# Kernel optimization log

Measured on AMD Instinct MI355X. Metric: run time of the kernel, lower is better.

## Reference

```python
import jax, jax.numpy as jnp
import numpy as np

HID = 768          # args.hidden_size
LSTM2 = 768        # args.lstm_dim * 2
SCALE = HID ** -0.5


def _cross_attn(q_in, kv_in, Wq, bq, Wk, bk, Wv, bv):
    # Linear projections (weights stored as [in, out])
    Q = q_in @ Wq + bq            # [B, Sq, H]
    K = kv_in @ Wk + bk           # [B, Sk, H]
    V = kv_in @ Wv + bv           # [B, Sk, H]
    attn = jnp.einsum('bqh,bkh->bqk', Q, K) * SCALE
    attn = jax.nn.softmax(attn, axis=-1)
    return jnp.einsum('bqk,bkh->bqh', attn, V)


def setup_inputs() -> dict:
    key = jax.random.key(0)
    ks = jax.random.split(key, 14)
    B, Ssyn, Ssem = 4, 4096, 2048
    syntactic_feat = jax.random.normal(ks[0], (B, Ssyn, LSTM2), jnp.float32)
    semantic_feat = jax.random.normal(ks[1], (B, Ssem, HID), jnp.float32)

    def lin(k, fan_in, fan_out):
        kw, kb = jax.random.split(k)
        bound = 1.0 / np.sqrt(fan_in)
        W = jax.random.uniform(kw, (fan_in, fan_out), jnp.float32, -bound, bound)
        b = jax.random.uniform(kb, (fan_out,), jnp.float32, -bound, bound)
        return W, b

    # syntax_to_semantic: query_dim=HID, key_dim=LSTM2
    Wq1, bq1 = lin(ks[2], HID, HID)
    Wk1, bk1 = lin(ks[3], LSTM2, HID)
    Wv1, bv1 = lin(ks[4], LSTM2, HID)
    # semantic_to_syntax: query_dim=LSTM2, key_dim=HID
    Wq2, bq2 = lin(ks[5], LSTM2, HID)
    Wk2, bk2 = lin(ks[6], HID, HID)
    Wv2, bv2 = lin(ks[7], HID, HID)
    return dict(syntactic_feat=syntactic_feat, semantic_feat=semantic_feat,
                Wq1=Wq1, bq1=bq1, Wk1=Wk1, bk1=bk1, Wv1=Wv1, bv1=bv1,
                Wq2=Wq2, bq2=bq2, Wk2=Wk2, bk2=bk2, Wv2=Wv2, bv2=bv2)


def reference(syntactic_feat, semantic_feat,
              Wq1, bq1, Wk1, bk1, Wv1, bv1,
              Wq2, bq2, Wk2, bk2, Wv2, bv2):
    # enhanced_semantic: queries from semantic, keys/values from syntactic
    enhanced_semantic = _cross_attn(semantic_feat, syntactic_feat,
                                    Wq1, bq1, Wk1, bk1, Wv1, bv1)
    # enhanced_syntax: queries from syntactic, keys/values from semantic
    enhanced_syntax = _cross_attn(syntactic_feat, semantic_feat,
                                  Wq2, bq2, Wk2, bk2, Wv2, bv2)
    return enhanced_semantic, enhanced_syntax
```

## Files before the change

kernel.cpp:

```cpp
#include <hip/hip_runtime.h>
#include <stdint.h>


typedef unsigned short u16;
typedef __attribute__((ext_vector_type(8))) __bf16 bf16x8;
typedef __attribute__((ext_vector_type(4))) float f32x4;

__device__ __forceinline__ float bf2f(u16 u) {
  union { unsigned int i; float f; } x; x.i = ((unsigned int)u) << 16; return x.f;
}
__device__ __forceinline__ u16 f2bf(float f) {
  union { float f; unsigned int i; } x; x.f = f;
  unsigned int i = x.i;
  i += 0x7fffu + ((i >> 16) & 1u);
  return (u16)(i >> 16);
}

__device__ __forceinline__ void cp16(void* lds, const void* g) {
  __builtin_amdgcn_global_load_lds((__attribute__((address_space(1))) void*)g,
                                   (__attribute__((address_space(3))) void*)lds,
                                   16, 0, 0);
}

template <int BIAS_MODE, int OUTF>
__global__ __launch_bounds__(256)
void gemm_bt_kernel(const u16* __restrict__ A, const u16* __restrict__ Bt,
                    const float* __restrict__ bias, void* __restrict__ Cv,
                    int K, int lda, int ldb, int ldc,
                    long sAb, long sBb, long sCb, float scale)
{
  __shared__ __align__(16) u16 Asl[128 * 32];
  __shared__ __align__(16) u16 Bsl[128 * 32];

  const int tid  = threadIdx.x;
  const int lane = tid & 63;
  const int wave = tid >> 6;
  const int l15  = lane & 15;
  const int quad = lane >> 4;
  const int mw   = (wave >> 1) * 64;
  const int nw   = (wave & 1) * 64;

  const long zb = blockIdx.z;
  const char* Ab = (const char*)(A + zb * sAb + (long)blockIdx.x * 128 * lda);
  const char* Bb = (const char*)(Bt + zb * sBb + (long)blockIdx.y * 128 * ldb);

  const int o   = wave * 1024 + lane * 16;
  const int mst = o >> 6;
  const int off = o & 63;
  char* ldsA = (char*)Asl + wave * 1024;
  char* ldsB = (char*)Bsl + wave * 1024;
  const long ldaB = (long)lda * 2;
  const long ldbB = (long)ldb * 2;
  const char* pa0 = Ab + (long)mst * ldaB + off;
  const char* pb0 = Bb + (long)mst * ldbB + off;

  f32x4 acc[4][4];
  {
    f32x4 zz = {0.f, 0.f, 0.f, 0.f};
#pragma unroll
    for (int i = 0; i < 4; ++i)
#pragma unroll
      for (int j = 0; j < 4; ++j) acc[i][j] = zz;
  }

  const int nk = K >> 5;
  for (int kk = 0; kk < nk; ++kk) {
    const long kb = (long)kk << 6;
    cp16(ldsA,        pa0 + kb);
    cp16(ldsA + 4096, pa0 + kb + 64 * ldaB);
    cp16(ldsB,        pb0 + kb);
    cp16(ldsB + 4096, pb0 + kb + 64 * ldbB);
    __syncthreads();

    bf16x8 a[4], b[4];
    const bf16x8* As8 = (const bf16x8*)Asl;
    const bf16x8* Bs8 = (const bf16x8*)Bsl;
#pragma unroll
    for (int i = 0; i < 4; ++i) a[i] = As8[(mw + i * 16 + l15) * 4 + quad];
#pragma unroll
    for (int j = 0; j < 4; ++j) b[j] = Bs8[(nw + j * 16 + l15) * 4 + quad];
#pragma unroll
    for (int i = 0; i < 4; ++i)
#pragma unroll
      for (int j = 0; j < 4; ++j)
        acc[i][j] = __builtin_amdgcn_mfma_f32_16x16x32_bf16(a[i], b[j], acc[i][j], 0, 0, 0);
    __syncthreads();
  }

  const int brow = blockIdx.x * 128 + mw + quad * 4;
  const int bcol = blockIdx.y * 128 + nw + l15;
  float cb[4];
  if (BIAS_MODE == 1) {
#pragma unroll
    for (int j = 0; j < 4; ++j) cb[j] = bias[bcol + j * 16];
  }
#pragma unroll
  for (int i = 0; i < 4; ++i) {
    const int r0 = brow + i * 16;
    float rb[4];
    if (BIAS_MODE == 2) {
#pragma unroll
      for (int r = 0; r < 4; ++r) rb[r] = bias[r0 + r];
    }
#pragma unroll
    for (int j = 0; j < 4; ++j) {
      const int col = bcol + j * 16;
#pragma unroll
      for (int r = 0; r < 4; ++r) {
        float x = acc[i][j][r] * scale;
        if (BIAS_MODE == 1) x += cb[j];
        if (BIAS_MODE == 2) x += rb[r];
        if (OUTF)
          ((float*)Cv)[zb * sCb + (long)(r0 + r) * ldc + col] = x;
        else
          ((u16*)Cv)[zb * sCb + (long)(r0 + r) * ldc + col] = f2bf(x);
      }
    }
  }
}

__global__ __launch_bounds__(256)
void cvt_bf16_kernel(const float* __restrict__ src, u16* __restrict__ dst, int n8)
{
  int idx = blockIdx.x * 256 + threadIdx.x;
  if (idx >= n8) return;
  const float4* s4 = (const float4*)src;
  float4 a = s4[idx * 2], b = s4[idx * 2 + 1];
  uint4 o;
  o.x = (unsigned int)f2bf(a.x) | ((unsigned int)f2bf(a.y) << 16);
  o.y = (unsigned int)f2bf(a.z) | ((unsigned int)f2bf(a.w) << 16);
  o.z = (unsigned int)f2bf(b.x) | ((unsigned int)f2bf(b.y) << 16);
  o.w = (unsigned int)f2bf(b.z) | ((unsigned int)f2bf(b.w) << 16);
  ((uint4*)dst)[idx] = o;
}

__global__ void transpose6_kernel(const float* s0, const float* s1, const float* s2,
                                  const float* s3, const float* s4, const float* s5,
                                  u16* d0, u16* d1, u16* d2,
                                  u16* d3, u16* d4, u16* d5)
{
  __shared__ float t[32][33];
  const float* src; u16* dst;
  switch (blockIdx.z) {
    case 0: src = s0; dst = d0; break;
    case 1: src = s1; dst = d1; break;
    case 2: src = s2; dst = d2; break;
    case 3: src = s3; dst = d3; break;
    case 4: src = s4; dst = d4; break;
    default: src = s5; dst = d5; break;
  }
  const int tx = threadIdx.x, ty = threadIdx.y;
  const int x = blockIdx.x * 32 + tx;
  const int y0 = blockIdx.y * 32;
#pragma unroll
  for (int j = 0; j < 32; j += 8) t[ty + j][tx] = src[(long)(y0 + ty + j) * 768 + x];
  __syncthreads();
  const int x2 = y0 + tx;
#pragma unroll
  for (int j = 0; j < 32; j += 8)
    dst[(long)(blockIdx.x * 32 + ty + j) * 768 + x2] = f2bf(t[tx][ty + j]);
}

template <int NV>
__global__ __launch_bounds__(256)
void softmax_kernel(u16* S)
{
  __shared__ float red[8];
  const int tid  = threadIdx.x;
  const int lane = tid & 63;
  const int wave = tid >> 6;
  uint4* p4 = (uint4*)(S + (long)blockIdx.x * (NV * 256));

  uint4 ld[NV / 8];
#pragma unroll
  for (int c = 0; c < NV / 8; ++c) ld[c] = p4[tid + c * 256];
  float v[NV];
#pragma unroll
  for (int c = 0; c < NV / 8; ++c) {
    unsigned int w[4] = {ld[c].x, ld[c].y, ld[c].z, ld[c].w};
#pragma unroll
    for (int q = 0; q < 4; ++q) {
      v[c * 8 + q * 2]     = bf2f((u16)(w[q] & 0xffffu));
      v[c * 8 + q * 2 + 1] = bf2f((u16)(w[q] >> 16));
    }
  }

  float m = -1e30f;
#pragma unroll
  for (int i = 0; i < NV; ++i) m = fmaxf(m, v[i]);
#pragma unroll
  for (int off = 32; off > 0; off >>= 1) m = fmaxf(m, __shfl_xor(m, off, 64));
  if (lane == 0) red[wave] = m;
  __syncthreads();
  m = fmaxf(fmaxf(red[0], red[1]), fmaxf(red[2], red[3]));

  float s = 0.f;
#pragma unroll
  for (int i = 0; i < NV; ++i) { v[i] = __expf(v[i] - m); s += v[i]; }
#pragma unroll
  for (int off = 32; off > 0; off >>= 1) s += __shfl_xor(s, off, 64);
  if (lane == 0) red[4 + wave] = s;
  __syncthreads();
  s = (red[4] + red[5]) + (red[6] + red[7]);
  const float inv = 1.0f / s;

#pragma unroll
  for (int c = 0; c < NV / 8; ++c) {
    unsigned int w[4];
#pragma unroll
    for (int q = 0; q < 4; ++q) {
      const u16 lo = f2bf(v[c * 8 + q * 2] * inv);
      const u16 hi = f2bf(v[c * 8 + q * 2 + 1] * inv);
      w[q] = (unsigned int)lo | ((unsigned int)hi << 16);
    }
    uint4 st; st.x = w[0]; st.y = w[1]; st.z = w[2]; st.w = w[3];
    p4[tid + c * 256] = st;
  }
}


static void launch_gemm(hipStream_t st, int mode, int outf,
                        const void* A, const void* Bt, const float* bias, void* C,
                        int M, int N, int K, int lda, int ldb, int ldc,
                        long sA, long sB, long sC, int nb, float scale)
{
  dim3 g(M / 128, N / 128, nb), b(256, 1, 1);
  const u16* Au = (const u16*)A;
  const u16* Bu = (const u16*)Bt;
  if (outf == 0) {
    if (mode == 0)
      gemm_bt_kernel<0, 0><<<g, b, 0, st>>>(Au, Bu, bias, C, K, lda, ldb, ldc, sA, sB, sC, scale);
    else if (mode == 1)
      gemm_bt_kernel<1, 0><<<g, b, 0, st>>>(Au, Bu, bias, C, K, lda, ldb, ldc, sA, sB, sC, scale);
    else
      gemm_bt_kernel<2, 0><<<g, b, 0, st>>>(Au, Bu, bias, C, K, lda, ldb, ldc, sA, sB, sC, scale);
  } else {
    if (mode == 0)
      gemm_bt_kernel<0, 1><<<g, b, 0, st>>>(Au, Bu, bias, C, K, lda, ldb, ldc, sA, sB, sC, scale);
    else if (mode == 1)
      gemm_bt_kernel<1, 1><<<g, b, 0, st>>>(Au, Bu, bias, C, K, lda, ldb, ldc, sA, sB, sC, scale);
    else
      gemm_bt_kernel<2, 1><<<g, b, 0, st>>>(Au, Bu, bias, C, K, lda, ldb, ldc, sA, sB, sC, scale);
  }
}

extern "C" void kernel_launch(void* const* d_in, const int* in_sizes, int n_in,
                              void* d_out, int out_size, void* d_ws, size_t ws_size,
                              hipStream_t stream)
{
  (void)in_sizes; (void)n_in; (void)out_size; (void)ws_size;
  const float* syn = (const float*)d_in[0];
  const float* sem = (const float*)d_in[1];
  const float* W[6]    = {(const float*)d_in[2], (const float*)d_in[4],  (const float*)d_in[6],
                          (const float*)d_in[8], (const float*)d_in[10], (const float*)d_in[12]};
  const float* bias[6] = {(const float*)d_in[3], (const float*)d_in[5],  (const float*)d_in[7],
                          (const float*)d_in[9], (const float*)d_in[11], (const float*)d_in[13]};
  float* out = (float*)d_out;

  u16* ws   = (u16*)d_ws;
  u16* WT   = ws;
  u16* synb = ws + 3538944;
  u16* semb = synb + 12582912;
  u16* bufA = semb + 6291456;
  u16* bufB = bufA + 12582912;
  u16* bufC = bufB + 12582912;
  u16* S    = bufC + 6291456;

  const float SC = 0.036084391824351615f;

  cvt_bf16_kernel<<<dim3(6144), dim3(256), 0, stream>>>(syn, synb, 1572864);
  cvt_bf16_kernel<<<dim3(3072), dim3(256), 0, stream>>>(sem, semb, 786432);
  transpose6_kernel<<<dim3(24, 24, 6), dim3(32, 8, 1), 0, stream>>>(
      W[0], W[1], W[2], W[3], W[4], W[5],
      WT + 0 * 589824, WT + 1 * 589824, WT + 2 * 589824,
      WT + 3 * 589824, WT + 4 * 589824, WT + 5 * 589824);

  launch_gemm(stream, 1, 0, synb, WT + 1 * 589824, bias[1], bufA,
              16384, 768, 768, 768, 768, 768, 0, 0, 0, 1, 1.f);
  launch_gemm(stream, 2, 0, WT + 2 * 589824, synb, bias[2], bufB,
              768, 16384, 768, 768, 768, 16384, 0, 0, 0, 1, 1.f);
  launch_gemm(stream, 1, 0, semb, WT + 0 * 589824, bias[0], bufC,
              8192, 768, 768, 768, 768, 768, 0, 0, 0, 1, 1.f);
  launch_gemm(stream, 0, 0, bufC, bufA, nullptr, S,
              2048, 4096, 768, 768, 768, 4096,
              2048L * 768, 4096L * 768, 2048L * 4096, 4, SC);
  softmax_kernel<16><<<dim3(8192), dim3(256), 0, stream>>>(S);
  launch_gemm(stream, 0, 1, S, bufB, nullptr, out,
              2048, 768, 4096, 4096, 16384, 768,
              2048L * 4096, 4096L, 2048L * 768, 4, 1.f);

  launch_gemm(stream, 1, 0, synb, WT + 3 * 589824, bias[3], bufA,
              16384, 768, 768, 768, 768, 768, 0, 0, 0, 1, 1.f);
  launch_gemm(stream, 1, 0, semb, WT + 4 * 589824, bias[4], bufC,
              8192, 768, 768, 768, 768, 768, 0, 0, 0, 1, 1.f);
  launch_gemm(stream, 2, 0, WT + 5 * 589824, semb, bias[5], bufB,
              768, 8192, 768, 768, 768, 8192, 0, 0, 0, 1, 1.f);
  launch_gemm(stream, 0, 0, bufA, bufC, nullptr, S,
              4096, 2048, 768, 768, 768, 2048,
              4096L * 768, 2048L * 768, 4096L * 2048, 4, SC);
  softmax_kernel<8><<<dim3(16384), dim3(256), 0, stream>>>(S);
  launch_gemm(stream, 0, 1, S, bufB, nullptr, out + 6291456,
              4096, 768, 2048, 2048, 8192, 768,
              4096L * 2048, 2048L, 4096L * 768, 4, 1.f);
}
```

Before: 703.6 us.

## Batch independent GEMMs into grouped multi-descriptor launches and merge conversion kernels

Replaces the templated GEMM with a grouped kernel that reads a pack of GEMM descriptors and maps a flat block index to the right problem. All six projections go in one launch, the second attention's QK^T shares a launch with the first attention's PV GEMM, and the two fp32-to-bf16 conversions are fused into one kernel. Workspace is reshuffled, and some intermediates are staged in the output buffer. The goal is fewer launches and better fill of the GPU with small GEMMs. In exchange, bias mode and output type become runtime branches instead of template parameters, which may add register pressure or instructions.

```diff
diff --git a/kernel.cpp b/kernel.cpp
--- a/kernel.cpp
+++ b/kernel.cpp
@@ -22,15 +22,34 @@
                                    16, 0, 0);
 }
 
-template <int BIAS_MODE, int OUTF>
+struct GemmDesc {
+  const u16* A; const u16* Bt; const float* bias; void* C;
+  long sA, sB, sC;
+  int K, lda, ldb, ldc;
+  int gx, gy;
+  int start;
+  int mode, outf;
+  float scale;
+};
+struct GemmPack { GemmDesc d[6]; int nd; };
+
 __global__ __launch_bounds__(256)
-void gemm_bt_kernel(const u16* __restrict__ A, const u16* __restrict__ Bt,
-                    const float* __restrict__ bias, void* __restrict__ Cv,
-                    int K, int lda, int ldb, int ldc,
-                    long sAb, long sBb, long sCb, float scale)
+void gemm_multi_kernel(GemmPack p)
 {
   __shared__ __align__(16) u16 Asl[128 * 32];
   __shared__ __align__(16) u16 Bsl[128 * 32];
+
+  int seg = 0;
+#pragma unroll
+  for (int t = 1; t < 6; ++t)
+    if (t < p.nd && (int)blockIdx.x >= p.d[t].start) seg = t;
+  const GemmDesc& g = p.d[seg];
+  const int local = (int)blockIdx.x - g.start;
+  const int pxy = g.gx * g.gy;
+  const int bz = local / pxy;
+  const int rem = local - bz * pxy;
+  const int by = rem / g.gx;
+  const int bx = rem - by * g.gx;
 
   const int tid  = threadIdx.x;
   const int lane = tid & 63;
@@ -40,17 +59,16 @@
   const int mw   = (wave >> 1) * 64;
   const int nw   = (wave & 1) * 64;
 
-  const long zb = blockIdx.z;
-  const char* Ab = (const char*)(A + zb * sAb + (long)blockIdx.x * 128 * lda);
-  const char* Bb = (const char*)(Bt + zb * sBb + (long)blockIdx.y * 128 * ldb);
+  const char* Ab = (const char*)(g.A + (long)bz * g.sA + (long)bx * 128 * g.lda);
+  const char* Bb = (const char*)(g.Bt + (long)bz * g.sB + (long)by * 128 * g.ldb);
 
   const int o   = wave * 1024 + lane * 16;
   const int mst = o >> 6;
   const int off = o & 63;
   char* ldsA = (char*)Asl + wave * 1024;
   char* ldsB = (char*)Bsl + wave * 1024;
-  const long ldaB = (long)lda * 2;
-  const long ldbB = (long)ldb * 2;
+  const long ldaB = (long)g.lda * 2;
+  const long ldbB = (long)g.ldb * 2;
   const char* pa0 = Ab + (long)mst * ldaB + off;
   const char* pb0 = Bb + (long)mst * ldbB + off;
 
@@ -63,7 +81,7 @@
       for (int j = 0; j < 4; ++j) acc[i][j] = zz;
   }
 
-  const int nk = K >> 5;
+  const int nk = g.K >> 5;
   for (int kk = 0; kk < nk; ++kk) {
     const long kb = (long)kk << 6;
     cp16(ldsA,        pa0 + kb);
@@ -87,51 +105,53 @@
     __syncthreads();
   }
 
-  const int brow = blockIdx.x * 128 + mw + quad * 4;
-  const int bcol = blockIdx.y * 128 + nw + l15;
+  const int brow = bx * 128 + mw + quad * 4;
+  const int bcol = by * 128 + nw + l15;
   float cb[4];
-  if (BIAS_MODE == 1) {
-#pragma unroll
-    for (int j = 0; j < 4; ++j) cb[j] = bias[bcol + j * 16];
+  if (g.mode == 1) {
+#pragma unroll
+    for (int j = 0; j < 4; ++j) cb[j] = g.bias[bcol + j * 16];
   }
 #pragma unroll
   for (int i = 0; i < 4; ++i) {
     const int r0 = brow + i * 16;
     float rb[4];
-    if (BIAS_MODE == 2) {
-#pragma unroll
-      for (int r = 0; r < 4; ++r) rb[r] = bias[r0 + r];
+    if (g.mode == 2) {
+#pragma unroll
+      for (int r = 0; r < 4; ++r) rb[r] = g.bias[r0 + r];
     }
 #pragma unroll
     for (int j = 0; j < 4; ++j) {
       const int col = bcol + j * 16;
 #pragma unroll
       for (int r = 0; r < 4; ++r) {
-        float x = acc[i][j][r] * scale;
-        if (BIAS_MODE == 1) x += cb[j];
-        if (BIAS_MODE == 2) x += rb[r];
-        if (OUTF)
-          ((float*)Cv)[zb * sCb + (long)(r0 + r) * ldc + col] = x;
-        else
-          ((u16*)Cv)[zb * sCb + (long)(r0 + r) * ldc + col] = f2bf(x);
+        float x = acc[i][j][r] * g.scale;
+        if (g.mode == 1) x += cb[j];
+        if (g.mode == 2) x += rb[r];
+        const long idx = (long)bz * g.sC + (long)(r0 + r) * g.ldc + col;
+        if (g.outf) ((float*)g.C)[idx] = x;
+        else        ((u16*)g.C)[idx] = f2bf(x);
       }
     }
   }
 }
 
 __global__ __launch_bounds__(256)
-void cvt_bf16_kernel(const float* __restrict__ src, u16* __restrict__ dst, int n8)
+void cvt2_bf16_kernel(const float* __restrict__ sa, u16* __restrict__ da, int n8a,
+                      const float* __restrict__ sb, u16* __restrict__ db, int n8b)
 {
   int idx = blockIdx.x * 256 + threadIdx.x;
-  if (idx >= n8) return;
+  const float* src; u16* dst; int i;
+  if (idx < n8a) { src = sa; dst = da; i = idx; }
+  else           { src = sb; dst = db; i = idx - n8a; if (i >= n8b) return; }
   const float4* s4 = (const float4*)src;
-  float4 a = s4[idx * 2], b = s4[idx * 2 + 1];
+  float4 a = s4[i * 2], b = s4[i * 2 + 1];
   uint4 o;
   o.x = (unsigned int)f2bf(a.x) | ((unsigned int)f2bf(a.y) << 16);
   o.y = (unsigned int)f2bf(a.z) | ((unsigned int)f2bf(a.w) << 16);
   o.z = (unsigned int)f2bf(b.x) | ((unsigned int)f2bf(b.y) << 16);
   o.w = (unsigned int)f2bf(b.z) | ((unsigned int)f2bf(b.w) << 16);
-  ((uint4*)dst)[idx] = o;
+  ((uint4*)dst)[i] = o;
 }
 
 __global__ void transpose6_kernel(const float* s0, const float* s1, const float* s2,
@@ -219,29 +239,18 @@
 }
 
 
-static void launch_gemm(hipStream_t st, int mode, int outf,
-                        const void* A, const void* Bt, const float* bias, void* C,
-                        int M, int N, int K, int lda, int ldb, int ldc,
-                        long sA, long sB, long sC, int nb, float scale)
-{
-  dim3 g(M / 128, N / 128, nb), b(256, 1, 1);
-  const u16* Au = (const u16*)A;
-  const u16* Bu = (const u16*)Bt;
-  if (outf == 0) {
-    if (mode == 0)
-      gemm_bt_kernel<0, 0><<<g, b, 0, st>>>(Au, Bu, bias, C, K, lda, ldb, ldc, sA, sB, sC, scale);
-    else if (mode == 1)
-      gemm_bt_kernel<1, 0><<<g, b, 0, st>>>(Au, Bu, bias, C, K, lda, ldb, ldc, sA, sB, sC, scale);
-    else
-      gemm_bt_kernel<2, 0><<<g, b, 0, st>>>(Au, Bu, bias, C, K, lda, ldb, ldc, sA, sB, sC, scale);
-  } else {
-    if (mode == 0)
-      gemm_bt_kernel<0, 1><<<g, b, 0, st>>>(Au, Bu, bias, C, K, lda, ldb, ldc, sA, sB, sC, scale);
-    else if (mode == 1)
-      gemm_bt_kernel<1, 1><<<g, b, 0, st>>>(Au, Bu, bias, C, K, lda, ldb, ldc, sA, sB, sC, scale);
-    else
-      gemm_bt_kernel<2, 1><<<g, b, 0, st>>>(Au, Bu, bias, C, K, lda, ldb, ldc, sA, sB, sC, scale);
-  }
+static GemmDesc mkdesc(const void* A, const void* Bt, const float* bias, void* C,
+                       long sA, long sB, long sC, int K, int lda, int ldb, int ldc,
+                       int M, int N, int nb, int start, int mode, int outf, float scale)
+{
+  GemmDesc d;
+  d.A = (const u16*)A; d.Bt = (const u16*)Bt; d.bias = bias; d.C = C;
+  d.sA = sA; d.sB = sB; d.sC = sC;
+  d.K = K; d.lda = lda; d.ldb = ldb; d.ldc = ldc;
+  d.gx = M / 128; d.gy = N / 128; d.start = start;
+  d.mode = mode; d.outf = outf; d.scale = scale;
+  (void)nb;
+  return d;
 }
 
 extern "C" void kernel_launch(void* const* d_in, const int* in_sizes, int n_in,
@@ -260,46 +269,71 @@
   u16* ws   = (u16*)d_ws;
   u16* WT   = ws;
   u16* synb = ws + 3538944;
-  u16* semb = synb + 12582912;
-  u16* bufA = semb + 6291456;
-  u16* bufB = bufA + 12582912;
-  u16* bufC = bufB + 12582912;
-  u16* S    = bufC + 6291456;
+  u16* semb = ws + 16121856;
+  u16* S1   = ws;
+  u16* K1   = ws + 33554432;
+  u16* Q1   = ws + 46137344;
+  u16* S2   = ws + 33554432;
+  u16* V1T  = ws + 67108864;
+  u16* V2T  = ws + 79691776;
+  u16* Q2   = (u16*)(out + 6291456);
+  u16* K2   = Q2 + 12582912;
 
   const float SC = 0.036084391824351615f;
 
-  cvt_bf16_kernel<<<dim3(6144), dim3(256), 0, stream>>>(syn, synb, 1572864);
-  cvt_bf16_kernel<<<dim3(3072), dim3(256), 0, stream>>>(sem, semb, 786432);
+  cvt2_bf16_kernel<<<dim3(9216), dim3(256), 0, stream>>>(
+      syn, synb, 1572864, sem, semb, 786432);
+
   transpose6_kernel<<<dim3(24, 24, 6), dim3(32, 8, 1), 0, stream>>>(
       W[0], W[1], W[2], W[3], W[4], W[5],
       WT + 0 * 589824, WT + 1 * 589824, WT + 2 * 589824,
       WT + 3 * 589824, WT + 4 * 589824, WT + 5 * 589824);
 
-  launch_gemm(stream, 1, 0, synb, WT + 1 * 589824, bias[1], bufA,
-              16384, 768, 768, 768, 768, 768, 0, 0, 0, 1, 1.f);
-  launch_gemm(stream, 2, 0, WT + 2 * 589824, synb, bias[2], bufB,
-              768, 16384, 768, 768, 768, 16384, 0, 0, 0, 1, 1.f);
-  launch_gemm(stream, 1, 0, semb, WT + 0 * 589824, bias[0], bufC,
-              8192, 768, 768, 768, 768, 768, 0, 0, 0, 1, 1.f);
-  launch_gemm(stream, 0, 0, bufC, bufA, nullptr, S,
-              2048, 4096, 768, 768, 768, 4096,
-              2048L * 768, 4096L * 768, 2048L * 4096, 4, SC);
-  softmax_kernel<16><<<dim3(8192), dim3(256), 0, stream>>>(S);
-  launch_gemm(stream, 0, 1, S, bufB, nullptr, out,
-              2048, 768, 4096, 4096, 16384, 768,
-              2048L * 4096, 4096L, 2048L * 768, 4, 1.f);
-
-  launch_gemm(stream, 1, 0, synb, WT + 3 * 589824, bias[3], bufA,
-              16384, 768, 768, 768, 768, 768, 0, 0, 0, 1, 1.f);
-  launch_gemm(stream, 1, 0, semb, WT + 4 * 589824, bias[4], bufC,
-              8192, 768, 768, 768, 768, 768, 0, 0, 0, 1, 1.f);
-  launch_gemm(stream, 2, 0, WT + 5 * 589824, semb, bias[5], bufB,
-              768, 8192, 768, 768, 768, 8192, 0, 0, 0, 1, 1.f);
-  launch_gemm(stream, 0, 0, bufA, bufC, nullptr, S,
-              4096, 2048, 768, 768, 768, 2048,
-              4096L * 768, 2048L * 768, 4096L * 2048, 4, SC);
-  softmax_kernel<8><<<dim3(16384), dim3(256), 0, stream>>>(S);
-  launch_gemm(stream, 0, 1, S, bufB, nullptr, out + 6291456,
-              4096, 768, 2048, 2048, 8192, 768,
-              4096L * 2048, 2048L, 4096L * 768, 4, 1.f);
-}
+  {
+    GemmPack p; p.nd = 6;
+    p.d[0] = mkdesc(synb, WT + 1 * 589824, bias[1], K1, 0, 0, 0,
+                    768, 768, 768, 768, 16384, 768, 1, 0, 1, 0, 1.f);
+    p.d[1] = mkdesc(synb, WT + 3 * 589824, bias[3], Q2, 0, 0, 0,
+                    768, 768, 768, 768, 16384, 768, 1, 768, 1, 0, 1.f);
+    p.d[2] = mkdesc(WT + 2 * 589824, synb, bias[2], V1T, 0, 0, 0,
+                    768, 768, 768, 16384, 768, 16384, 1, 1536, 2, 0, 1.f);
+    p.d[3] = mkdesc(semb, WT + 0 * 589824, bias[0], Q1, 0, 0, 0,
+                    768, 768, 768, 768, 8192, 768, 1, 2304, 1, 0, 1.f);
+    p.d[4] = mkdesc(semb, WT + 4 * 589824, bias[4], K2, 0, 0, 0,
+                    768, 768, 768, 768, 8192, 768, 1, 2688, 1, 0, 1.f);
+    p.d[5] = mkdesc(WT + 5 * 589824, semb, bias[5], V2T, 0, 0, 0,
+                    768, 768, 768, 8192, 768, 8192, 1, 3072, 2, 0, 1.f);
+    gemm_multi_kernel<<<dim3(3456), dim3(256), 0, stream>>>(p);
+  }
+
+  {
+    GemmPack p; p.nd = 1;
+    p.d[0] = mkdesc(Q1, K1, nullptr, S1,
+                    1572864L, 3145728L, 8388608L,
+                    768, 768, 768, 4096, 2048, 4096, 4, 0, 0, 0, SC);
+    gemm_multi_kernel<<<dim3(2048), dim3(256), 0, stream>>>(p);
+  }
+
+  softmax_kernel<16><<<dim3(8192), dim3(256), 0, stream>>>(S1);
+
+  {
+    GemmPack p; p.nd = 2;
+    p.d[0] = mkdesc(S1, V1T, nullptr, out,
+                    8388608L, 4096L, 1572864L,
+                    4096, 4096, 16384, 768, 2048, 768, 4, 0, 0, 1, 1.f);
+    p.d[1] = mkdesc(Q2, K2, nullptr, S2,
+                    3145728L, 1572864L, 8388608L,
+                    768, 768, 768, 2048, 4096, 2048, 4, 384, 0, 0, SC);
+    gemm_multi_kernel<<<dim3(2432), dim3(256), 0, stream>>>(p);
+  }
+
+  softmax_kernel<8><<<dim3(16384), dim3(256), 0, stream>>>(S2);
+
+  {
+    GemmPack p; p.nd = 1;
+    p.d[0] = mkdesc(S2, V2T, nullptr, out + 6291456,
+                    8388608L, 2048L, 3145728L,
+                    2048, 2048, 8192, 768, 4096, 768, 4, 0, 0, 1, 1.f);
+    gemm_multi_kernel<<<dim3(768), dim3(256), 0, stream>>>(p);
+  }
+}
```

New measurement: 650.3 us. 7.6% less time.
